# Optimization experiments

Measured on AMD Instinct MI355X. Metric: run time of the kernel, lower is better.

## Reference

```python
import jax, jax.numpy as jnp
import numpy as np

DIM = 2048
N_HEADS = 16
N_KV_HEADS = 4
HEAD_DIM = DIM // N_HEADS  # 128
B, S = 2, 2048


def setup_inputs() -> dict:
    key = jax.random.key(0)
    ks = jax.random.split(key, 7)
    x = jax.random.normal(ks[0], (B, S, DIM), dtype=jnp.float32)
    # rotary tables: freqs_cis = exp(i * t * theta), theta_j = 1/10000^(2j/head_dim)
    inv_freq = 1.0 / (10000.0 ** (np.arange(0, HEAD_DIM, 2, dtype=np.float32) / HEAD_DIM))
    t = np.arange(S, dtype=np.float32)
    angles = jnp.asarray(np.outer(t, inv_freq))  # [S, HEAD_DIM//2]
    freqs_cos = jnp.cos(angles)
    freqs_sin = jnp.sin(angles)
    # Linear weights stored [in, out] (torch Linear applies x @ W.T; equivalent math)
    sd = 1.0 / np.sqrt(DIM)
    wq = jax.random.uniform(ks[1], (DIM, N_HEADS * HEAD_DIM), jnp.float32, -sd, sd)
    wk = jax.random.uniform(ks[2], (DIM, N_KV_HEADS * HEAD_DIM), jnp.float32, -sd, sd)
    wv = jax.random.uniform(ks[3], (DIM, N_KV_HEADS * HEAD_DIM), jnp.float32, -sd, sd)
    wo = jax.random.uniform(ks[4], (N_HEADS * HEAD_DIM, DIM), jnp.float32, -sd, sd)
    return {"x": x, "freqs_cos": freqs_cos, "freqs_sin": freqs_sin,
            "wq": wq, "wk": wk, "wv": wv, "wo": wo}


def _apply_rotary(xq, xk, cos, sin):
    # xq: [B,S,H,D], xk: [B,S,KH,D]; cos/sin: [S, D//2]
    def rot(t):
        tr = t.reshape(*t.shape[:-1], -1, 2)  # [..., D//2, 2] (real, imag)
        r, i = tr[..., 0], tr[..., 1]
        c = cos[None, :, None, :]
        s = sin[None, :, None, :]
        out_r = r * c - i * s
        out_i = r * s + i * c
        return jnp.stack([out_r, out_i], axis=-1).reshape(t.shape)
    return rot(xq), rot(xk)


def reference(x, freqs_cos, freqs_sin, wq, wk, wv, wo):
    bsz, seqlen, _ = x.shape
    xq = (x @ wq).reshape(bsz, seqlen, N_HEADS, HEAD_DIM)
    xk = (x @ wk).reshape(bsz, seqlen, N_KV_HEADS, HEAD_DIM)
    xv = (x @ wv).reshape(bsz, seqlen, N_KV_HEADS, HEAD_DIM)
    xq, xk = _apply_rotary(xq, xk, freqs_cos, freqs_sin)
    rep = N_HEADS // N_KV_HEADS
    xk = jnp.repeat(xk, rep, axis=2)
    xv = jnp.repeat(xv, rep, axis=2)
    # [B,H,S,D]
    q = xq.transpose(0, 2, 1, 3)
    k = xk.transpose(0, 2, 1, 3)
    v = xv.transpose(0, 2, 1, 3)
    scale = 1.0 / jnp.sqrt(jnp.asarray(HEAD_DIM, dtype=q.dtype))
    scores = jnp.einsum('bhqd,bhkd->bhqk', q, k) * scale
    causal = jnp.tril(jnp.ones((seqlen, seqlen), dtype=bool))
    scores = jnp.where(causal[None, None], scores, jnp.asarray(-jnp.inf, scores.dtype))
    attn = jax.nn.softmax(scores, axis=-1)
    out = jnp.einsum('bhqk,bhkd->bhqd', attn, v)  # [B,H,S,D]
    out = out.transpose(0, 2, 1, 3).reshape(bsz, seqlen, N_HEADS * HEAD_DIM)
    return out @ wo
```

## Files before the change

### kernel.cpp

```cpp
#include <hip/hip_runtime.h>
#include <hip/hip_bf16.h>

typedef unsigned short u16;
typedef unsigned int u32;
typedef __bf16 bf16x8 __attribute__((ext_vector_type(8)));
typedef float f32x4 __attribute__((ext_vector_type(4)));
typedef u32 u32x2 __attribute__((ext_vector_type(2)));

#define AS1 __attribute__((address_space(1)))
#define AS3 __attribute__((address_space(3)))

__device__ __forceinline__ void gload16(const void* gp, void* lp) {
    __builtin_amdgcn_global_load_lds((const AS1 u32*)gp, (AS3 u32*)lp, 16, 0, 0);
}

__device__ __forceinline__ u16 f2b(float f) {
    __bf16 h = (__bf16)f;
    return __builtin_bit_cast(u16, h);
}

__global__ __launch_bounds__(256) void prep_kernel(const float* __restrict__ x,
                                                   const float* __restrict__ wq,
                                                   const float* __restrict__ wk,
                                                   const float* __restrict__ wv,
                                                   const float* __restrict__ wo,
                                                   u16* __restrict__ xb,
                                                   u16* __restrict__ wT,
                                                   u16* __restrict__ woT) {
    __shared__ u16 tile[32][33];
    const int bid = blockIdx.x, tid = threadIdx.x;
    if (bid < 8192) {
        int i = bid * 256 + tid;
        f32x4 v = *(const f32x4*)(x + (size_t)i * 4);
        u32x2 o;
        o[0] = (u32)f2b(v[0]) | ((u32)f2b(v[1]) << 16);
        o[1] = (u32)f2b(v[2]) | ((u32)f2b(v[3]) << 16);
        *(u32x2*)(xb + (size_t)i * 4) = o;
        return;
    }
    const float* in;
    u16* out;
    int C, t;
    if (bid < 12288) { t = bid - 8192; in = wq; out = wT; C = 2048; }
    else if (bid < 13312) { t = bid - 12288; in = wk; out = wT + 2048 * 2048; C = 512; }
    else if (bid < 14336) { t = bid - 13312; in = wv; out = wT + 2560 * 2048; C = 512; }
    else { t = bid - 14336; in = wo; out = woT; C = 2048; }
    const int nbx = C >> 5;
    const int bx = (t % nbx) * 32, by = (t / nbx) * 32;
    const int tx = tid & 31, ty = tid >> 5;
#pragma unroll
    for (int i = 0; i < 32; i += 8)
        tile[ty + i][tx] = f2b(in[(size_t)(by + ty + i) * C + bx + tx]);
    __syncthreads();
#pragma unroll
    for (int i = 0; i < 32; i += 8)
        out[(size_t)(bx + ty + i) * 2048 + by + tx] = tile[tx][ty + i];
}

__global__ __launch_bounds__(256) void transpose_v(const u16* __restrict__ qkv,
                                                   u16* __restrict__ vT) {
    __shared__ u16 tile[32][33];
    const int bx = blockIdx.x * 32;
    const int by = blockIdx.y * 32;
    const int tx = threadIdx.x & 31, ty = threadIdx.x >> 5;
#pragma unroll
    for (int i = 0; i < 32; i += 8)
        tile[ty + i][tx] = qkv[(size_t)(by + ty + i) * 3072 + 2560 + bx + tx];
    __syncthreads();
    const int b = by >> 11, s0 = by & 2047;
#pragma unroll
    for (int i = 0; i < 32; i += 8)
        vT[(size_t)(b * 512 + bx + ty + i) * 2048 + s0 + tx] = tile[tx][ty + i];
}

template <typename OT, bool ROPE>
__global__ __launch_bounds__(256) void gemm_bt(const __bf16* __restrict__ A,
                                               const __bf16* __restrict__ Bt,
                                               OT* __restrict__ C,
                                               int K, int ldc,
                                               const float* __restrict__ fc,
                                               const float* __restrict__ fs) {
    __shared__ __align__(16) __bf16 Al[128 * 32];
    __shared__ __align__(16) __bf16 Bl[128 * 32];
    const int tid = threadIdx.x;
    const int lane = tid & 63, w = tid >> 6;
    const int wm = w >> 1, wn = w & 1;
    const int ln15 = lane & 15, lg = lane >> 4;
    const int nwg = gridDim.x * gridDim.y;
    const int lid = blockIdx.y * gridDim.x + blockIdx.x;
    const int swz = (lid & 7) * (nwg >> 3) + (lid >> 3);
    const int bm = swz / gridDim.x, bn = swz % gridDim.x;

    const f32x4 fzero = {0.f, 0.f, 0.f, 0.f};
    f32x4 acc[4][4];
#pragma unroll
    for (int m = 0; m < 4; m++)
#pragma unroll
        for (int n = 0; n < 4; n++) acc[m][n] = fzero;

    const __bf16* Ab = A + (size_t)(bm * 128) * K;
    const __bf16* Bb = Bt + (size_t)(bn * 128) * K;

    for (int k0 = 0; k0 < K; k0 += 32) {
#pragma unroll
        for (int i = 0; i < 2; i++) {
            int gid = i * 256 + tid;
            int row = gid >> 2, gc = gid & 3;
            gload16(Ab + (size_t)row * K + k0 + gc * 8, (char*)Al + gid * 16);
            gload16(Bb + (size_t)row * K + k0 + gc * 8, (char*)Bl + gid * 16);
        }
        __syncthreads();
        bf16x8 af[4], bfr[4];
#pragma unroll
        for (int m = 0; m < 4; m++)
            af[m] = *(const bf16x8*)&Al[(wm * 64 + m * 16 + ln15) * 32 + lg * 8];
#pragma unroll
        for (int n = 0; n < 4; n++)
            bfr[n] = *(const bf16x8*)&Bl[(wn * 64 + n * 16 + ln15) * 32 + lg * 8];
#pragma unroll
        for (int m = 0; m < 4; m++)
#pragma unroll
            for (int n = 0; n < 4; n++)
                acc[m][n] = __builtin_amdgcn_mfma_f32_16x16x32_bf16(af[m], bfr[n], acc[m][n], 0, 0, 0);
        __syncthreads();
    }

    if (ROPE) {
#pragma unroll
        for (int n = 0; n < 4; n++) {
            const int col = bn * 128 + wn * 64 + n * 16 + ln15;
            if (col < 2560) {
                const int p = (col & 127) >> 1;
                const bool odd = (col & 1) != 0;
#pragma unroll
                for (int m = 0; m < 4; m++)
#pragma unroll
                    for (int r = 0; r < 4; r++) {
                        const int row = bm * 128 + wm * 64 + m * 16 + lg * 4 + r;
                        const int sp = row & 2047;
                        float c = fc[sp * 64 + p];
                        float sn = fs[sp * 64 + p];
                        float v = acc[m][n][r];
                        float v2 = __shfl_xor(v, 1);
                        acc[m][n][r] = odd ? (v2 * sn + v * c) : (v * c - v2 * sn);
                    }
            }
        }
    }

#pragma unroll
    for (int m = 0; m < 4; m++)
#pragma unroll
        for (int n = 0; n < 4; n++)
#pragma unroll
            for (int r = 0; r < 4; r++) {
                int row = bm * 128 + wm * 64 + m * 16 + lg * 4 + r;
                int col = bn * 128 + wn * 64 + n * 16 + ln15;
                C[(size_t)row * ldc + col] = (OT)acc[m][n][r];
            }
}

__global__ __launch_bounds__(256, 2) void attn_kernel(const __bf16* __restrict__ qkv,
                                                      const __bf16* __restrict__ vT,
                                                      __bf16* __restrict__ ctx) {
    __shared__ __align__(16) __bf16 Klds[2][64 * 128];
    __shared__ __align__(16) __bf16 VTlds[2][128 * 64];
    __shared__ __align__(16) __bf16 Plds[4][16 * 64];

    const int tid = threadIdx.x, lane = tid & 63, w = tid >> 6;
    const int ln15 = lane & 15, lg = lane >> 4;
    int i = blockIdx.x, qblk, hb;
    if (i < 256) { qblk = 15 - (i >> 5); hb = i & 31; }
    else { int j = i - 256; qblk = j >> 5; hb = j & 31; }
    const int h = hb >> 1, b = hb & 1;
    const int kvh = h >> 2;
    const int q0 = qblk * 128;
    const int qw0 = q0 + w * 32;
    const float c1 = 0.08838834764831845f * 1.4426950408889634f;

    const __bf16* qbase = qkv + (size_t)(b * 2048 + qw0 + ln15) * 3072 + h * 128;
    bf16x8 aq[2][4];
#pragma unroll
    for (int m = 0; m < 2; m++)
#pragma unroll
        for (int c = 0; c < 4; c++)
            aq[m][c] = *(const bf16x8*)(qbase + (size_t)m * 16 * 3072 + c * 32 + lg * 8);

    const __bf16* Kg = qkv + (size_t)(b * 2048) * 3072 + 2048 + kvh * 128;
    const __bf16* Vg = vT + (size_t)((b * 4 + kvh) * 128) * 2048;

    const f32x4 fzero = {0.f, 0.f, 0.f, 0.f};
    float m_run[2][4], l_run[2][4];
    f32x4 acc[2][8];
#pragma unroll
    for (int m = 0; m < 2; m++)
#pragma unroll
        for (int r = 0; r < 4; r++) { m_run[m][r] = -1e30f; l_run[m][r] = 0.f; }
#pragma unroll
    for (int m = 0; m < 2; m++)
#pragma unroll
        for (int dt = 0; dt < 8; dt++) acc[m][dt] = fzero;

    const int nt = 2 * qblk + 2;

#define STAGE(buf, t)                                                                     \
    do {                                                                                  \
        const int kb_ = (t) * 64;                                                         \
        _Pragma("unroll") for (int i2 = 0; i2 < 4; i2++) {                                \
            int gid = i2 * 256 + tid;                                                     \
            int kv = gid >> 4, sl = gid & 15;                                             \
            gload16(Kg + (size_t)(kb_ + kv) * 3072 + ((sl ^ (kv & 7)) * 8),               \
                    (char*)Klds[buf] + gid * 16);                                         \
        }                                                                                 \
        _Pragma("unroll") for (int i2 = 0; i2 < 4; i2++) {                                \
            int gid = i2 * 256 + tid;                                                     \
            int d = gid >> 3, sl = gid & 7;                                               \
            gload16(Vg + (size_t)d * 2048 + kb_ + ((sl ^ (d & 7)) * 8),                   \
                    (char*)VTlds[buf] + gid * 16);                                        \
        }                                                                                 \
    } while (0)

    STAGE(0, 0);
    __syncthreads();

    for (int t = 0; t < nt; t++) {
        const int cur = t & 1;
        const int kbase = t * 64;
        if (t + 1 < nt) STAGE(cur ^ 1, t + 1);

        if (kbase <= qw0 + 31) {
            f32x4 st[2][4];
#pragma unroll
            for (int ct = 0; ct < 4; ct++) {
                int kv = ct * 16 + ln15;
                f32x4 s0 = fzero, s1 = fzero;
#pragma unroll
                for (int c = 0; c < 4; c++) {
                    int g = c * 4 + lg;
                    bf16x8 bk = *(const bf16x8*)&Klds[cur][kv * 128 + ((g ^ (kv & 7)) * 8)];
                    s0 = __builtin_amdgcn_mfma_f32_16x16x32_bf16(aq[0][c], bk, s0, 0, 0, 0);
                    s1 = __builtin_amdgcn_mfma_f32_16x16x32_bf16(aq[1][c], bk, s1, 0, 0, 0);
                }
                st[0][ct] = s0;
                st[1][ct] = s1;
            }
            if (kbase + 63 > qw0) {
#pragma unroll
                for (int m = 0; m < 2; m++)
#pragma unroll
                    for (int ct = 0; ct < 4; ct++) {
                        int kvi = kbase + ct * 16 + ln15;
#pragma unroll
                        for (int r = 0; r < 4; r++) {
                            int qi = qw0 + m * 16 + lg * 4 + r;
                            if (kvi > qi) st[m][ct][r] = -1e30f;
                        }
                    }
            }
#pragma unroll
            for (int m = 0; m < 2; m++) {
#pragma unroll
                for (int r = 0; r < 4; r++) {
                    float m0 = fmaxf(fmaxf(st[m][0][r], st[m][1][r]), fmaxf(st[m][2][r], st[m][3][r]));
#pragma unroll
                    for (int off = 1; off < 16; off <<= 1) m0 = fmaxf(m0, __shfl_xor(m0, off, 16));
                    float mn = fmaxf(m_run[m][r], m0);
                    float corr = exp2f((m_run[m][r] - mn) * c1);
                    m_run[m][r] = mn;
                    const int q = lg * 4 + r;
                    float sm = 0.f;
#pragma unroll
                    for (int ct = 0; ct < 4; ct++) {
                        float p = exp2f((st[m][ct][r] - mn) * c1);
                        sm += p;
                        int pg = ct * 2 + (ln15 >> 3);
                        Plds[w][q * 64 + ((pg ^ (q & 7)) * 8) + (ln15 & 7)] = (__bf16)p;
                    }
#pragma unroll
                    for (int off = 1; off < 16; off <<= 1) sm += __shfl_xor(sm, off, 16);
                    l_run[m][r] = l_run[m][r] * corr + sm;
#pragma unroll
                    for (int dt = 0; dt < 8; dt++) acc[m][dt][r] *= corr;
                }
#pragma unroll
                for (int s2 = 0; s2 < 2; s2++) {
                    const int kvg = s2 * 4 + lg;
                    bf16x8 pa = *(const bf16x8*)&Plds[w][ln15 * 64 + ((kvg ^ (ln15 & 7)) * 8)];
#pragma unroll
                    for (int dt = 0; dt < 8; dt++) {
                        int d = dt * 16 + ln15;
                        bf16x8 bv = *(const bf16x8*)&VTlds[cur][d * 64 + ((kvg ^ (d & 7)) * 8)];
                        acc[m][dt] = __builtin_amdgcn_mfma_f32_16x16x32_bf16(pa, bv, acc[m][dt], 0, 0, 0);
                    }
                }
            }
        }
        __syncthreads();
    }
#undef STAGE

    __bf16* crow = ctx + (size_t)(b * 2048 + qw0) * 2048 + h * 128;
#pragma unroll
    for (int m = 0; m < 2; m++)
#pragma unroll
        for (int dt = 0; dt < 8; dt++)
#pragma unroll
            for (int r = 0; r < 4; r++) {
                float v = acc[m][dt][r] / l_run[m][r];
                crow[(size_t)(m * 16 + lg * 4 + r) * 2048 + dt * 16 + ln15] = (__bf16)v;
            }
}

extern "C" void kernel_launch(void* const* d_in, const int* in_sizes, int n_in,
                              void* d_out, int out_size, void* d_ws, size_t ws_size,
                              hipStream_t stream) {
    const float* x = (const float*)d_in[0];
    const float* fc = (const float*)d_in[1];
    const float* fs = (const float*)d_in[2];
    const float* wq = (const float*)d_in[3];
    const float* wk = (const float*)d_in[4];
    const float* wv = (const float*)d_in[5];
    const float* wo = (const float*)d_in[6];
    float* out = (float*)d_out;

    char* ws = (char*)d_ws;
    __bf16* wT  = (__bf16*)ws;
    __bf16* woT = (__bf16*)(ws + 12582912);
    __bf16* xb  = (__bf16*)(ws + 20971520);
    __bf16* qkv = (__bf16*)(ws + 37748736);
    __bf16* ctx = (__bf16*)(ws + 62914560);
    __bf16* vT  = xb;

    prep_kernel<<<18432, 256, 0, stream>>>(x, wq, wk, wv, wo, (u16*)xb, (u16*)wT, (u16*)woT);

    gemm_bt<__bf16, true><<<dim3(24, 32), 256, 0, stream>>>(xb, wT, qkv, 2048, 3072, fc, fs);

    transpose_v<<<dim3(16, 128), 256, 0, stream>>>((const u16*)qkv, (u16*)vT);

    attn_kernel<<<512, 256, 0, stream>>>(qkv, vT, ctx);

    gemm_bt<float, false><<<dim3(16, 32), 256, 0, stream>>>(ctx, woT, out, 2048, 2048, nullptr, nullptr);
}
```

Before: 410.3 us.

## Single-buffer K tile, batch softmax reductions, and interleave PV MFMAs

The K tile in LDS goes from double-buffered to single-buffered. An extra barrier after QK^T lets the next tile's K and V loads be issued mid-iteration, which cuts LDS use and lets the compiler choose occupancy freely. Softmax max and sum shuffle reductions are batched across all 8 rows to expose ILP. The P tile for both 16-row halves is written to LDS first, so the PV MFMAs for both halves share each V fragment load. The extra barrier per iteration and less prefetch lead time are the risks, and dropping the occupancy hint in launch bounds may change register allocation.

Result: slower. 448.5 us (+9.3%).

```diff
diff --git a/kernel.cpp b/kernel.cpp
--- a/kernel.cpp
+++ b/kernel.cpp
@@ -160,12 +160,12 @@
             }
 }
 
-__global__ __launch_bounds__(256, 2) void attn_kernel(const __bf16* __restrict__ qkv,
-                                                      const __bf16* __restrict__ vT,
-                                                      __bf16* __restrict__ ctx) {
-    __shared__ __align__(16) __bf16 Klds[2][64 * 128];
+__global__ __launch_bounds__(256) void attn_kernel(const __bf16* __restrict__ qkv,
+                                                   const __bf16* __restrict__ vT,
+                                                   __bf16* __restrict__ ctx) {
+    __shared__ __align__(16) __bf16 Klds[64 * 128];
     __shared__ __align__(16) __bf16 VTlds[2][128 * 64];
-    __shared__ __align__(16) __bf16 Plds[4][16 * 64];
+    __shared__ __align__(16) __bf16 Plds[4][32 * 64];
 
     const int tid = threadIdx.x, lane = tid & 63, w = tid >> 6;
     const int ln15 = lane & 15, lg = lane >> 4;
@@ -174,8 +174,7 @@
     else { int j = i - 256; qblk = j >> 5; hb = j & 31; }
     const int h = hb >> 1, b = hb & 1;
     const int kvh = h >> 2;
-    const int q0 = qblk * 128;
-    const int qw0 = q0 + w * 32;
+    const int qw0 = qblk * 128 + w * 32;
     const float c1 = 0.08838834764831845f * 1.4426950408889634f;
 
     const __bf16* qbase = qkv + (size_t)(b * 2048 + qw0 + ln15) * 3072 + h * 128;
@@ -190,28 +189,30 @@
     const __bf16* Vg = vT + (size_t)((b * 4 + kvh) * 128) * 2048;
 
     const f32x4 fzero = {0.f, 0.f, 0.f, 0.f};
-    float m_run[2][4], l_run[2][4];
+    float m_run[8], l_run[8];
     f32x4 acc[2][8];
 #pragma unroll
+    for (int i2 = 0; i2 < 8; i2++) { m_run[i2] = -1e30f; l_run[i2] = 0.f; }
+#pragma unroll
     for (int m = 0; m < 2; m++)
 #pragma unroll
-        for (int r = 0; r < 4; r++) { m_run[m][r] = -1e30f; l_run[m][r] = 0.f; }
-#pragma unroll
-    for (int m = 0; m < 2; m++)
-#pragma unroll
         for (int dt = 0; dt < 8; dt++) acc[m][dt] = fzero;
 
     const int nt = 2 * qblk + 2;
 
-#define STAGE(buf, t)                                                                     \
+#define STAGE_K(t)                                                                        \
     do {                                                                                  \
         const int kb_ = (t) * 64;                                                         \
         _Pragma("unroll") for (int i2 = 0; i2 < 4; i2++) {                                \
             int gid = i2 * 256 + tid;                                                     \
             int kv = gid >> 4, sl = gid & 15;                                             \
             gload16(Kg + (size_t)(kb_ + kv) * 3072 + ((sl ^ (kv & 7)) * 8),               \
-                    (char*)Klds[buf] + gid * 16);                                         \
+                    (char*)Klds + gid * 16);                                              \
         }                                                                                 \
+    } while (0)
+#define STAGE_V(buf, t)                                                                   \
+    do {                                                                                  \
+        const int kb_ = (t) * 64;                                                         \
         _Pragma("unroll") for (int i2 = 0; i2 < 4; i2++) {                                \
             int gid = i2 * 256 + tid;                                                     \
             int d = gid >> 3, sl = gid & 7;                                               \
@@ -220,16 +221,17 @@
         }                                                                                 \
     } while (0)
 
-    STAGE(0, 0);
+    STAGE_K(0);
+    STAGE_V(0, 0);
     __syncthreads();
 
+    int cur = 0;
     for (int t = 0; t < nt; t++) {
-        const int cur = t & 1;
         const int kbase = t * 64;
-        if (t + 1 < nt) STAGE(cur ^ 1, t + 1);
-
-        if (kbase <= qw0 + 31) {
-            f32x4 st[2][4];
+        const bool active = (kbase <= qw0 + 31);
+
+        f32x4 st[2][4];
+        if (active) {
 #pragma unroll
             for (int ct = 0; ct < 4; ct++) {
                 int kv = ct * 16 + ln15;
@@ -237,13 +239,18 @@
 #pragma unroll
                 for (int c = 0; c < 4; c++) {
                     int g = c * 4 + lg;
-                    bf16x8 bk = *(const bf16x8*)&Klds[cur][kv * 128 + ((g ^ (kv & 7)) * 8)];
+                    bf16x8 bk = *(const bf16x8*)&Klds[kv * 128 + ((g ^ (kv & 7)) * 8)];
                     s0 = __builtin_amdgcn_mfma_f32_16x16x32_bf16(aq[0][c], bk, s0, 0, 0, 0);
                     s1 = __builtin_amdgcn_mfma_f32_16x16x32_bf16(aq[1][c], bk, s1, 0, 0, 0);
                 }
                 st[0][ct] = s0;
                 st[1][ct] = s1;
             }
+        }
+        __syncthreads();
+        if (t + 1 < nt) { STAGE_K(t + 1); STAGE_V(cur ^ 1, t + 1); }
+
+        if (active) {
             if (kbase + 63 > qw0) {
 #pragma unroll
                 for (int m = 0; m < 2; m++)
@@ -257,47 +264,74 @@
                         }
                     }
             }
-#pragma unroll
-            for (int m = 0; m < 2; m++) {
+            float tm[8];
+#pragma unroll
+            for (int m = 0; m < 2; m++)
+#pragma unroll
+                for (int r = 0; r < 4; r++)
+                    tm[m * 4 + r] = fmaxf(fmaxf(st[m][0][r], st[m][1][r]),
+                                          fmaxf(st[m][2][r], st[m][3][r]));
+#pragma unroll
+            for (int off = 1; off < 16; off <<= 1)
+#pragma unroll
+                for (int i2 = 0; i2 < 8; i2++)
+                    tm[i2] = fmaxf(tm[i2], __shfl_xor(tm[i2], off, 16));
+            float corr[8];
+#pragma unroll
+            for (int i2 = 0; i2 < 8; i2++) {
+                float mn = fmaxf(m_run[i2], tm[i2]);
+                corr[i2] = exp2f((m_run[i2] - mn) * c1);
+                m_run[i2] = mn;
+            }
+            float ts[8];
+#pragma unroll
+            for (int m = 0; m < 2; m++)
 #pragma unroll
                 for (int r = 0; r < 4; r++) {
-                    float m0 = fmaxf(fmaxf(st[m][0][r], st[m][1][r]), fmaxf(st[m][2][r], st[m][3][r]));
-#pragma unroll
-                    for (int off = 1; off < 16; off <<= 1) m0 = fmaxf(m0, __shfl_xor(m0, off, 16));
-                    float mn = fmaxf(m_run[m][r], m0);
-                    float corr = exp2f((m_run[m][r] - mn) * c1);
-                    m_run[m][r] = mn;
-                    const int q = lg * 4 + r;
-                    float sm = 0.f;
+                    const int i2 = m * 4 + r;
+                    const int q = m * 16 + lg * 4 + r;
+                    float s = 0.f;
 #pragma unroll
                     for (int ct = 0; ct < 4; ct++) {
-                        float p = exp2f((st[m][ct][r] - mn) * c1);
-                        sm += p;
+                        float p = exp2f((st[m][ct][r] - m_run[i2]) * c1);
+                        s += p;
                         int pg = ct * 2 + (ln15 >> 3);
                         Plds[w][q * 64 + ((pg ^ (q & 7)) * 8) + (ln15 & 7)] = (__bf16)p;
                     }
-#pragma unroll
-                    for (int off = 1; off < 16; off <<= 1) sm += __shfl_xor(sm, off, 16);
-                    l_run[m][r] = l_run[m][r] * corr + sm;
-#pragma unroll
-                    for (int dt = 0; dt < 8; dt++) acc[m][dt][r] *= corr;
+                    ts[i2] = s;
                 }
 #pragma unroll
-                for (int s2 = 0; s2 < 2; s2++) {
-                    const int kvg = s2 * 4 + lg;
-                    bf16x8 pa = *(const bf16x8*)&Plds[w][ln15 * 64 + ((kvg ^ (ln15 & 7)) * 8)];
-#pragma unroll
-                    for (int dt = 0; dt < 8; dt++) {
-                        int d = dt * 16 + ln15;
-                        bf16x8 bv = *(const bf16x8*)&VTlds[cur][d * 64 + ((kvg ^ (d & 7)) * 8)];
-                        acc[m][dt] = __builtin_amdgcn_mfma_f32_16x16x32_bf16(pa, bv, acc[m][dt], 0, 0, 0);
-                    }
+            for (int off = 1; off < 16; off <<= 1)
+#pragma unroll
+                for (int i2 = 0; i2 < 8; i2++)
+                    ts[i2] += __shfl_xor(ts[i2], off, 16);
+#pragma unroll
+            for (int i2 = 0; i2 < 8; i2++) l_run[i2] = l_run[i2] * corr[i2] + ts[i2];
+#pragma unroll
+            for (int m = 0; m < 2; m++)
+#pragma unroll
+                for (int dt = 0; dt < 8; dt++)
+#pragma unroll
+                    for (int r = 0; r < 4; r++) acc[m][dt][r] *= corr[m * 4 + r];
+#pragma unroll
+            for (int s2 = 0; s2 < 2; s2++) {
+                const int kvg = s2 * 4 + lg;
+                bf16x8 pa0 = *(const bf16x8*)&Plds[w][(0 * 16 + ln15) * 64 + ((kvg ^ (ln15 & 7)) * 8)];
+                bf16x8 pa1 = *(const bf16x8*)&Plds[w][(1 * 16 + ln15) * 64 + ((kvg ^ (ln15 & 7)) * 8)];
+#pragma unroll
+                for (int dt = 0; dt < 8; dt++) {
+                    int d = dt * 16 + ln15;
+                    bf16x8 bv = *(const bf16x8*)&VTlds[cur][d * 64 + ((kvg ^ (d & 7)) * 8)];
+                    acc[0][dt] = __builtin_amdgcn_mfma_f32_16x16x32_bf16(pa0, bv, acc[0][dt], 0, 0, 0);
+                    acc[1][dt] = __builtin_amdgcn_mfma_f32_16x16x32_bf16(pa1, bv, acc[1][dt], 0, 0, 0);
                 }
             }
         }
         __syncthreads();
+        cur ^= 1;
     }
-#undef STAGE
+#undef STAGE_K
+#undef STAGE_V
 
     __bf16* crow = ctx + (size_t)(b * 2048 + qw0) * 2048 + h * 128;
 #pragma unroll
@@ -306,7 +340,7 @@
         for (int dt = 0; dt < 8; dt++)
 #pragma unroll
             for (int r = 0; r < 4; r++) {
-                float v = acc[m][dt][r] / l_run[m][r];
+                float v = acc[m][dt][r] / l_run[m * 4 + r];
                 crow[(size_t)(m * 16 + lg * 4 + r) * 2048 + dt * 16 + ln15] = (__bf16)v;
             }
 }
```

## Use eight waves per attention block with 16 query rows each

Applied to the files above, without the earlier changes.

The attention kernel moves from 4 waves handling 32 query rows each to 8 waves handling 16 rows each, with 512 threads per block. Staging loads are split across twice as many threads and the P scratch buffer is doubled. The softmax reductions are also batched across the four rows so the shuffles can interleave. The aim is more latency hiding and lower register pressure per wave. In exchange, each K/V fragment read from LDS now feeds only one MFMA instead of two, which roughly doubles LDS traffic per FLOP.

New measurement: 399.5 us. 1.03x faster.

```diff
diff --git a/kernel.cpp b/kernel.cpp
--- a/kernel.cpp
+++ b/kernel.cpp
@@ -160,12 +160,12 @@
             }
 }
 
-__global__ __launch_bounds__(256, 2) void attn_kernel(const __bf16* __restrict__ qkv,
-                                                      const __bf16* __restrict__ vT,
-                                                      __bf16* __restrict__ ctx) {
+__global__ __launch_bounds__(512) void attn_kernel(const __bf16* __restrict__ qkv,
+                                                   const __bf16* __restrict__ vT,
+                                                   __bf16* __restrict__ ctx) {
     __shared__ __align__(16) __bf16 Klds[2][64 * 128];
     __shared__ __align__(16) __bf16 VTlds[2][128 * 64];
-    __shared__ __align__(16) __bf16 Plds[4][16 * 64];
+    __shared__ __align__(16) __bf16 Plds[8][16 * 64];
 
     const int tid = threadIdx.x, lane = tid & 63, w = tid >> 6;
     const int ln15 = lane & 15, lg = lane >> 4;
@@ -174,46 +174,39 @@
     else { int j = i - 256; qblk = j >> 5; hb = j & 31; }
     const int h = hb >> 1, b = hb & 1;
     const int kvh = h >> 2;
-    const int q0 = qblk * 128;
-    const int qw0 = q0 + w * 32;
+    const int qw0 = qblk * 128 + w * 16;
     const float c1 = 0.08838834764831845f * 1.4426950408889634f;
 
     const __bf16* qbase = qkv + (size_t)(b * 2048 + qw0 + ln15) * 3072 + h * 128;
-    bf16x8 aq[2][4];
-#pragma unroll
-    for (int m = 0; m < 2; m++)
-#pragma unroll
-        for (int c = 0; c < 4; c++)
-            aq[m][c] = *(const bf16x8*)(qbase + (size_t)m * 16 * 3072 + c * 32 + lg * 8);
+    bf16x8 aq[4];
+#pragma unroll
+    for (int c = 0; c < 4; c++)
+        aq[c] = *(const bf16x8*)(qbase + c * 32 + lg * 8);
 
     const __bf16* Kg = qkv + (size_t)(b * 2048) * 3072 + 2048 + kvh * 128;
     const __bf16* Vg = vT + (size_t)((b * 4 + kvh) * 128) * 2048;
 
     const f32x4 fzero = {0.f, 0.f, 0.f, 0.f};
-    float m_run[2][4], l_run[2][4];
-    f32x4 acc[2][8];
-#pragma unroll
-    for (int m = 0; m < 2; m++)
-#pragma unroll
-        for (int r = 0; r < 4; r++) { m_run[m][r] = -1e30f; l_run[m][r] = 0.f; }
-#pragma unroll
-    for (int m = 0; m < 2; m++)
-#pragma unroll
-        for (int dt = 0; dt < 8; dt++) acc[m][dt] = fzero;
+    float m_run[4], l_run[4];
+    f32x4 acc[8];
+#pragma unroll
+    for (int r = 0; r < 4; r++) { m_run[r] = -1e30f; l_run[r] = 0.f; }
+#pragma unroll
+    for (int dt = 0; dt < 8; dt++) acc[dt] = fzero;
 
     const int nt = 2 * qblk + 2;
 
 #define STAGE(buf, t)                                                                     \
     do {                                                                                  \
         const int kb_ = (t) * 64;                                                         \
-        _Pragma("unroll") for (int i2 = 0; i2 < 4; i2++) {                                \
-            int gid = i2 * 256 + tid;                                                     \
+        _Pragma("unroll") for (int i2 = 0; i2 < 2; i2++) {                                \
+            int gid = i2 * 512 + tid;                                                     \
             int kv = gid >> 4, sl = gid & 15;                                             \
             gload16(Kg + (size_t)(kb_ + kv) * 3072 + ((sl ^ (kv & 7)) * 8),               \
                     (char*)Klds[buf] + gid * 16);                                         \
         }                                                                                 \
-        _Pragma("unroll") for (int i2 = 0; i2 < 4; i2++) {                                \
-            int gid = i2 * 256 + tid;                                                     \
+        _Pragma("unroll") for (int i2 = 0; i2 < 2; i2++) {                                \
+            int gid = i2 * 512 + tid;                                                     \
             int d = gid >> 3, sl = gid & 7;                                               \
             gload16(Vg + (size_t)d * 2048 + kb_ + ((sl ^ (d & 7)) * 8),                   \
                     (char*)VTlds[buf] + gid * 16);                                        \
@@ -228,70 +221,81 @@
         const int kbase = t * 64;
         if (t + 1 < nt) STAGE(cur ^ 1, t + 1);
 
-        if (kbase <= qw0 + 31) {
-            f32x4 st[2][4];
+        if (kbase <= qw0 + 15) {
+            f32x4 st[4];
 #pragma unroll
             for (int ct = 0; ct < 4; ct++) {
                 int kv = ct * 16 + ln15;
-                f32x4 s0 = fzero, s1 = fzero;
+                f32x4 s = fzero;
 #pragma unroll
                 for (int c = 0; c < 4; c++) {
                     int g = c * 4 + lg;
                     bf16x8 bk = *(const bf16x8*)&Klds[cur][kv * 128 + ((g ^ (kv & 7)) * 8)];
-                    s0 = __builtin_amdgcn_mfma_f32_16x16x32_bf16(aq[0][c], bk, s0, 0, 0, 0);
-                    s1 = __builtin_amdgcn_mfma_f32_16x16x32_bf16(aq[1][c], bk, s1, 0, 0, 0);
+                    s = __builtin_amdgcn_mfma_f32_16x16x32_bf16(aq[c], bk, s, 0, 0, 0);
                 }
-                st[0][ct] = s0;
-                st[1][ct] = s1;
+                st[ct] = s;
             }
             if (kbase + 63 > qw0) {
 #pragma unroll
-                for (int m = 0; m < 2; m++)
-#pragma unroll
-                    for (int ct = 0; ct < 4; ct++) {
-                        int kvi = kbase + ct * 16 + ln15;
-#pragma unroll
-                        for (int r = 0; r < 4; r++) {
-                            int qi = qw0 + m * 16 + lg * 4 + r;
-                            if (kvi > qi) st[m][ct][r] = -1e30f;
-                        }
+                for (int ct = 0; ct < 4; ct++) {
+                    int kvi = kbase + ct * 16 + ln15;
+#pragma unroll
+                    for (int r = 0; r < 4; r++) {
+                        int qi = qw0 + lg * 4 + r;
+                        if (kvi > qi) st[ct][r] = -1e30f;
                     }
-            }
-#pragma unroll
-            for (int m = 0; m < 2; m++) {
-#pragma unroll
-                for (int r = 0; r < 4; r++) {
-                    float m0 = fmaxf(fmaxf(st[m][0][r], st[m][1][r]), fmaxf(st[m][2][r], st[m][3][r]));
-#pragma unroll
-                    for (int off = 1; off < 16; off <<= 1) m0 = fmaxf(m0, __shfl_xor(m0, off, 16));
-                    float mn = fmaxf(m_run[m][r], m0);
-                    float corr = exp2f((m_run[m][r] - mn) * c1);
-                    m_run[m][r] = mn;
-                    const int q = lg * 4 + r;
-                    float sm = 0.f;
-#pragma unroll
-                    for (int ct = 0; ct < 4; ct++) {
-                        float p = exp2f((st[m][ct][r] - mn) * c1);
-                        sm += p;
-                        int pg = ct * 2 + (ln15 >> 3);
-                        Plds[w][q * 64 + ((pg ^ (q & 7)) * 8) + (ln15 & 7)] = (__bf16)p;
-                    }
-#pragma unroll
-                    for (int off = 1; off < 16; off <<= 1) sm += __shfl_xor(sm, off, 16);
-                    l_run[m][r] = l_run[m][r] * corr + sm;
-#pragma unroll
-                    for (int dt = 0; dt < 8; dt++) acc[m][dt][r] *= corr;
                 }
-#pragma unroll
-                for (int s2 = 0; s2 < 2; s2++) {
-                    const int kvg = s2 * 4 + lg;
-                    bf16x8 pa = *(const bf16x8*)&Plds[w][ln15 * 64 + ((kvg ^ (ln15 & 7)) * 8)];
-#pragma unroll
-                    for (int dt = 0; dt < 8; dt++) {
-                        int d = dt * 16 + ln15;
-                        bf16x8 bv = *(const bf16x8*)&VTlds[cur][d * 64 + ((kvg ^ (d & 7)) * 8)];
-                        acc[m][dt] = __builtin_amdgcn_mfma_f32_16x16x32_bf16(pa, bv, acc[m][dt], 0, 0, 0);
-                    }
+            }
+            float tm[4];
+#pragma unroll
+            for (int r = 0; r < 4; r++)
+                tm[r] = fmaxf(fmaxf(st[0][r], st[1][r]), fmaxf(st[2][r], st[3][r]));
+#pragma unroll
+            for (int off = 1; off < 16; off <<= 1)
+#pragma unroll
+                for (int r = 0; r < 4; r++)
+                    tm[r] = fmaxf(tm[r], __shfl_xor(tm[r], off, 16));
+            float corr[4];
+#pragma unroll
+            for (int r = 0; r < 4; r++) {
+                float mn = fmaxf(m_run[r], tm[r]);
+                corr[r] = exp2f((m_run[r] - mn) * c1);
+                m_run[r] = mn;
+            }
+            float ts[4];
+#pragma unroll
+            for (int r = 0; r < 4; r++) {
+                const int q = lg * 4 + r;
+                float s = 0.f;
+#pragma unroll
+                for (int ct = 0; ct < 4; ct++) {
+                    float p = exp2f((st[ct][r] - m_run[r]) * c1);
+                    s += p;
+                    int pg = ct * 2 + (ln15 >> 3);
+                    Plds[w][q * 64 + ((pg ^ (q & 7)) * 8) + (ln15 & 7)] = (__bf16)p;
+                }
+                ts[r] = s;
+            }
+#pragma unroll
+            for (int off = 1; off < 16; off <<= 1)
+#pragma unroll
+                for (int r = 0; r < 4; r++)
+                    ts[r] += __shfl_xor(ts[r], off, 16);
+#pragma unroll
+            for (int r = 0; r < 4; r++) l_run[r] = l_run[r] * corr[r] + ts[r];
+#pragma unroll
+            for (int dt = 0; dt < 8; dt++)
+#pragma unroll
+                for (int r = 0; r < 4; r++) acc[dt][r] *= corr[r];
+#pragma unroll
+            for (int s2 = 0; s2 < 2; s2++) {
+                const int kvg = s2 * 4 + lg;
+                bf16x8 pa = *(const bf16x8*)&Plds[w][ln15 * 64 + ((kvg ^ (ln15 & 7)) * 8)];
+#pragma unroll
+                for (int dt = 0; dt < 8; dt++) {
+                    int d = dt * 16 + ln15;
+                    bf16x8 bv = *(const bf16x8*)&VTlds[cur][d * 64 + ((kvg ^ (d & 7)) * 8)];
+                    acc[dt] = __builtin_amdgcn_mfma_f32_16x16x32_bf16(pa, bv, acc[dt], 0, 0, 0);
                 }
             }
         }
@@ -301,14 +305,12 @@
 
     __bf16* crow = ctx + (size_t)(b * 2048 + qw0) * 2048 + h * 128;
 #pragma unroll
-    for (int m = 0; m < 2; m++)
-#pragma unroll
-        for (int dt = 0; dt < 8; dt++)
-#pragma unroll
-            for (int r = 0; r < 4; r++) {
-                float v = acc[m][dt][r] / l_run[m][r];
-                crow[(size_t)(m * 16 + lg * 4 + r) * 2048 + dt * 16 + ln15] = (__bf16)v;
-            }
+    for (int dt = 0; dt < 8; dt++)
+#pragma unroll
+        for (int r = 0; r < 4; r++) {
+            float v = acc[dt][r] / l_run[r];
+            crow[(size_t)(lg * 4 + r) * 2048 + dt * 16 + ln15] = (__bf16)v;
+        }
 }
 
 extern "C" void kernel_launch(void* const* d_in, const int* in_sizes, int n_in,
@@ -337,7 +339,7 @@
 
     transpose_v<<<dim3(16, 128), 256, 0, stream>>>((const u16*)qkv, (u16*)vT);
 
-    attn_kernel<<<512, 256, 0, stream>>>(qkv, vT, ctx);
+    attn_kernel<<<512, 512, 0, stream>>>(qkv, vT, ctx);
 
     gemm_bt<float, false><<<dim3(16, 32), 256, 0, stream>>>(ctx, woT, out, 2048, 2048, nullptr, nullptr);
 }
```
